# Optimization experiments

Measured on AMD Instinct MI355X. Metric: run time of the kernel, lower is better.

Reference implementation:

```python
import jax, jax.numpy as jnp
import numpy as np

K = 3
STRIDE = 1
PADDING = 1


def _conv2d(x, w, b, stride, padding):
    out = jax.lax.conv_general_dilated(
        x, w, window_strides=(stride, stride),
        padding=[(padding, padding), (padding, padding)],
        dimension_numbers=('NCHW', 'OIHW', 'NCHW'))
    return out + b[None, :, None, None]


def _grid_sample_bilinear_zeros(x, grid):
    B, C, Hin, Win = x.shape
    gx = (grid[..., 0] + 1.0) * (Win * 0.5) - 0.5  # (B,Hg,Wg) pixel coords
    gy = (grid[..., 1] + 1.0) * (Hin * 0.5) - 0.5
    x0f = jnp.floor(gx)
    y0f = jnp.floor(gy)
    wx1 = gx - x0f  # bilinear weights
    wy1 = gy - y0f
    x0 = x0f.astype(jnp.int32)
    y0 = y0f.astype(jnp.int32)
    xf = x.reshape(B, C, Hin * Win)

    def gather(yi, xi):
        valid = (xi >= 0) & (xi < Win) & (yi >= 0) & (yi < Hin)  # zero padding
        idx = jnp.clip(yi, 0, Hin - 1) * Win + jnp.clip(xi, 0, Win - 1)
        g = jax.vmap(lambda xb, ib: xb[:, ib])(xf, idx)  # (B,C,Hg,Wg)
        return g * valid[:, None, :, :].astype(x.dtype)

    w00 = ((1.0 - wx1) * (1.0 - wy1))[:, None]
    w01 = (wx1 * (1.0 - wy1))[:, None]
    w10 = ((1.0 - wx1) * wy1)[:, None]
    w11 = (wx1 * wy1)[:, None]
    return (gather(y0, x0) * w00 + gather(y0, x0 + 1) * w01 +
            gather(y0 + 1, x0) * w10 + gather(y0 + 1, x0 + 1) * w11)


def setup_inputs() -> dict:
    key = jax.random.key(0)
    k1, k2, k3 = jax.random.split(key, 3)
    B, C, O, H, W = 8, 128, 128, 64, 64
    x = jax.random.normal(k1, (B, C, H, W), dtype=jnp.float32)
    # small offset-predictor weights so sampled locations stay near the grid
    w_off = jax.random.normal(k2, (2 * K * K, C, K, K), dtype=jnp.float32) * 1e-3
    b_off = jnp.zeros((2 * K * K,), dtype=jnp.float32)
    w_main = jax.random.normal(k3, (O, C, K, K), dtype=jnp.float32) * 0.05
    b_main = jnp.zeros((O,), dtype=jnp.float32)
    return {"x": x, "w_off": w_off, "b_off": b_off, "w_main": w_main, "b_main": b_main}


def reference(x, w_off, b_off, w_main, b_main):
    offset = _conv2d(x, w_off, b_off, STRIDE, PADDING)  # (B, 2*K*K, H, W)
    B, _, H, W = offset.shape
    off = jnp.transpose(offset, (0, 2, 3, 1)).reshape(B, H, W, K, K, 2)
    # The torch in-place loops reduce to:
    #   x-comp: cumsum over i of column j=0, broadcast over j
    #   y-comp: cumsum over j of row    i=0, broadcast over i
    ox = jnp.cumsum(off[:, :, :, :, 0, 0], axis=3)  # (B,H,W,K)
    oy = jnp.cumsum(off[:, :, :, 0, :, 1], axis=3)  # (B,H,W,K)
    ox_f = jnp.broadcast_to(ox[..., None], (B, H, W, K, K))
    oy_f = jnp.broadcast_to(oy[:, :, :, None, :], (B, H, W, K, K))
    off_f = jnp.stack([ox_f, oy_f], axis=-1).reshape(B, H, W, K * K, 2)

    y_range = jnp.linspace(-1.0, 1.0, H, dtype=x.dtype)
    x_range = jnp.linspace(-1.0, 1.0, W, dtype=x.dtype)
    yg, xg = jnp.meshgrid(y_range, x_range, indexing='ij')
    base = jnp.stack((xg, yg), axis=-1)  # (H,W,2)
    grid = base[None, :, :, None, :] + off_f  # (B,H,W,K*K,2)
    grid = grid.reshape(B, H, W * K * K, 2)

    xs = _grid_sample_bilinear_zeros(x, grid)  # (B,C,H,W*K*K)
    C = x.shape[1]
    xs = xs.reshape(B, C, H, W, K * K)
    wm = w_main.reshape(w_main.shape[0], C, K * K)
    out = jnp.einsum('bchwk,ock->bohw', xs, wm)
    return out + b_main[None, :, None, None]
```

## Files before the change

### kernel.cpp

```cpp
#include <hip/hip_runtime.h>
#include <hip/hip_bf16.h>
#include <stdint.h>

typedef unsigned short u16;
typedef unsigned int u32;
typedef __attribute__((ext_vector_type(8))) short short8;
typedef __attribute__((ext_vector_type(4))) float float4v;
typedef __attribute__((ext_vector_type(2))) float float2v;

#define CH 128
#define OO 128
#define KD 1152
#define MPIX 32768

__device__ __forceinline__ u16 f2bf(float v) {
    __hip_bfloat16 h = __float2bfloat16(v);
    return *reinterpret_cast<u16*>(&h);
}

__device__ __forceinline__ float bf_lo(u32 u) {
    u32 t = u << 16;
    return __builtin_bit_cast(float, t);
}
__device__ __forceinline__ float bf_hi(u32 u) {
    u32 t = u & 0xffff0000u;
    return __builtin_bit_cast(float, t);
}
__device__ __forceinline__ float2v unpk(u32 u) {
    float2v r;
    r.x = bf_lo(u);
    r.y = bf_hi(u);
    return r;
}
__device__ __forceinline__ u32 pack_bf16(float lo, float hi) {
    return (u32)f2bf(lo) | ((u32)f2bf(hi) << 16);
}

__global__ __launch_bounds__(256) void prep_kernel(const float* __restrict__ x,
                                                   const float* __restrict__ w_off,
                                                   const float* __restrict__ w_main,
                                                   __hip_bfloat16* __restrict__ xt,
                                                   float* __restrict__ partial,
                                                   u16* __restrict__ Wb) {
    __shared__ float st[64][65];
    int tid = threadIdx.x;
    int bid = blockIdx.x;

    if (bid < 512) {
        int bh = bid;
        int b = bh >> 6;
        int h = bh & 63;
        const float* xb = x + ((size_t)b * CH) * 4096 + (size_t)h * 64;
        u32* xo32 = (u32*)(xt + ((size_t)bh << 6) * CH);
        for (int cc0 = 0; cc0 < 128; cc0 += 64) {
            #pragma unroll
            for (int step = 0; step < 16; ++step) {
                int cl = (tid >> 6) + step * 4;
                int w = tid & 63;
                st[cl][w] = xb[(size_t)(cc0 + cl) * 4096 + w];
            }
            __syncthreads();
            #pragma unroll
            for (int step = 0; step < 8; ++step) {
                int w = (tid >> 5) + step * 8;
                int p = tid & 31;
                u32 pair = pack_bf16(st[2 * p][w], st[2 * p + 1][w]);
                xo32[(size_t)w * 64 + (cc0 >> 1) + p] = pair;
            }
            __syncthreads();
        }
    } else if (bid < 1024) {
        int idx = bid - 512;
        int m = (idx & 127) * 256 + tid;
        int chunk = idx >> 7;
        int b = m >> 12;
        int hw = m & 4095;
        int h = hw >> 6;
        int w = hw & 63;
        float acc[6] = {0.f, 0.f, 0.f, 0.f, 0.f, 0.f};
        int c0 = chunk * 32;
        for (int c = c0; c < c0 + 32; ++c) {
            const float* xc = x + ((size_t)(b * CH + c) << 12);
            float xv[9];
            #pragma unroll
            for (int dy = 0; dy < 3; ++dy) {
                int yy = h + dy - 1;
                bool vy = (unsigned)yy < 64u;
                #pragma unroll
                for (int dx = 0; dx < 3; ++dx) {
                    int xx = w + dx - 1;
                    bool vv = vy && ((unsigned)xx < 64u);
                    xv[dy * 3 + dx] = vv ? xc[yy * 64 + xx] : 0.f;
                }
            }
            const float* wb = w_off + (size_t)c * 9;
            #pragma unroll
            for (int s = 0; s < 6; ++s) {
                int chn = (s < 3) ? s * 6 : (s - 3) * 2 + 1;
                const float* wp = wb + (size_t)chn * (CH * 9);
                float a = acc[s];
                #pragma unroll
                for (int t = 0; t < 9; ++t) a = fmaf(xv[t], wp[t], a);
                acc[s] = a;
            }
        }
        float* po = partial + ((size_t)(chunk << 15) + m) * 6;
        #pragma unroll
        for (int s = 0; s < 6; ++s) po[s] = acc[s];
    } else {
        int idx = (bid - 1024) * 256 + tid;
        if (idx < OO * KD) {
            int o = idx / KD;
            int r = idx - o * KD;
            int k = r >> 7;
            int c = r & 127;
            Wb[idx] = f2bf(w_main[(size_t)o * KD + c * 9 + k]);
        }
    }
}

__global__ __launch_bounds__(256) void fused_gemm_kernel(const __hip_bfloat16* __restrict__ xt,
                                                         const float* __restrict__ partial,
                                                         const float* __restrict__ b_off,
                                                         const u16* __restrict__ Wb,
                                                         const float* __restrict__ b_main,
                                                         float* __restrict__ out) {
    __shared__ float offs[64][6];
    __shared__ __align__(16) float4v twt[64][9];
    __shared__ __align__(16) int4 tbs[64][9];
    __shared__ __align__(16) u16 lB[2][64 * 32];

    int tid = threadIdx.x;
    int orig = blockIdx.x;
    int b = orig & 7;
    int h = orig >> 3;
    int m0 = ((b << 6) + h) << 6;

    for (int idx = tid; idx < 64 * 6; idx += 256) {
        int pix = idx / 6, s = idx % 6;
        int m = m0 + pix;
        int chn = (s < 3) ? s * 6 : (s - 3) * 2 + 1;
        float v = b_off[chn];
        #pragma unroll
        for (int q = 0; q < 4; ++q) v += partial[((size_t)(q << 15) + m) * 6 + s];
        offs[pix][s] = v;
    }
    __syncthreads();

    for (int idx = tid; idx < 64 * 9; idx += 256) {
        int pix = idx / 9, k = idx % 9;
        int i = k / 3, j = k - i * 3;
        float ox = offs[pix][0];
        if (i >= 1) ox += offs[pix][1];
        if (i >= 2) ox += offs[pix][2];
        float oy = offs[pix][3];
        if (j >= 1) oy += offs[pix][4];
        if (j >= 2) oy += offs[pix][5];
        const float step = 2.0f / 63.0f;
        float bxn = -1.0f + pix * step;
        float byn = -1.0f + h * step;
        float gx = fmaf(bxn + ox, 32.0f, 31.5f);
        float gy = fmaf(byn + oy, 32.0f, 31.5f);
        float x0f = floorf(gx), y0f = floorf(gy);
        float wx = gx - x0f, wy = gy - y0f;
        int ix0 = (int)x0f, iy0 = (int)y0f;
        int ix1 = ix0 + 1, iy1 = iy0 + 1;
        float fx0 = ((unsigned)ix0 < 64u) ? 1.f : 0.f;
        float fx1 = ((unsigned)ix1 < 64u) ? 1.f : 0.f;
        float fy0 = ((unsigned)iy0 < 64u) ? 1.f : 0.f;
        float fy1 = ((unsigned)iy1 < 64u) ? 1.f : 0.f;
        float4v wv;
        wv[0] = (1.f - wy) * (1.f - wx) * fy0 * fx0;
        wv[1] = (1.f - wy) * wx * fy0 * fx1;
        wv[2] = wy * (1.f - wx) * fy1 * fx0;
        wv[3] = wy * wx * fy1 * fx1;
        int cx0 = min(max(ix0, 0), 63), cx1 = min(max(ix1, 0), 63);
        int cy0 = min(max(iy0, 0), 63), cy1 = min(max(iy1, 0), 63);
        twt[pix][k] = wv;
        tbs[pix][k] = make_int4((cy0 * 64 + cx0) * 64, (cy0 * 64 + cx1) * 64,
                                (cy1 * 64 + cx0) * 64, (cy1 * 64 + cx1) * 64);
    }
    __syncthreads();

    int wave = tid >> 6, lane = tid & 63;
    int wo = wave & 1;
    int wp = wave >> 1;
    int mrow = lane & 15;
    int q8 = (lane >> 4) * 8;

    int pix = tid >> 2;
    int cgp = (tid & 3) * 8;
    const u32* xb = (const u32*)(xt + (((size_t)b << 12) * (size_t)CH));
    const u16* arow = Wb + (size_t)(wo * 64 + mrow) * KD + q8;
    int bsto = pix * 32 + cgp;

    float4v acc[4][2];
    #pragma unroll
    for (int sm = 0; sm < 4; ++sm)
        #pragma unroll
        for (int sn = 0; sn < 2; ++sn)
            acc[sm][sn] = (float4v){0.f, 0.f, 0.f, 0.f};

    float4v wv;
    int4 bv;
    uint4 u00, u01, u10, u11;

    auto issueB = [&](int kk) {
        if ((kk & 3) == 0) {
            int k = kk >> 2;
            wv = twt[pix][k];
            bv = tbs[pix][k];
        }
        const u32* xc = xb + ((((kk & 3) << 5) + cgp) >> 1);
        u00 = *(const uint4*)(xc + bv.x);
        u01 = *(const uint4*)(xc + bv.y);
        u10 = *(const uint4*)(xc + bv.z);
        u11 = *(const uint4*)(xc + bv.w);
    };
    auto issueA = [&](int kk, uint4* dst) {
        const u16* ap = arow + kk * 32;
        #pragma unroll
        for (int s = 0; s < 4; ++s)
            dst[s] = *(const uint4*)(ap + (size_t)(s * 16) * KD);
    };

    auto dostep = [&](int kk, uint4* aC, uint4* aN) {
        u16* lBc = &lB[kk & 1][0];
        {
            const u32* p00 = (const u32*)&u00;
            const u32* p01 = (const u32*)&u01;
            const u32* p10 = (const u32*)&u10;
            const u32* p11 = (const u32*)&u11;
            u32 outp[4];
            #pragma unroll
            for (int q = 0; q < 4; ++q) {
                float2v p = unpk(p00[q]) * wv[0];
                p += unpk(p01[q]) * wv[1];
                p += unpk(p10[q]) * wv[2];
                p += unpk(p11[q]) * wv[3];
                outp[q] = pack_bf16(p.x, p.y);
            }
            *(uint4*)&lBc[bsto] = *(const uint4*)outp;
        }

        if (kk < 35) {
            issueB(kk + 1);
            issueA(kk + 1, aN);
        }

        __syncthreads();

        short8 bfv[2];
        #pragma unroll
        for (int s = 0; s < 2; ++s)
            bfv[s] = *(const short8*)&lBc[(wp * 32 + s * 16 + mrow) * 32 + q8];
        #pragma unroll
        for (int sm = 0; sm < 4; ++sm) {
            short8 af = __builtin_bit_cast(short8, aC[sm]);
            #pragma unroll
            for (int sn = 0; sn < 2; ++sn)
                acc[sm][sn] = __builtin_amdgcn_mfma_f32_16x16x32_bf16(af, bfv[sn],
                                                                     acc[sm][sn], 0, 0, 0);
        }
    };

    uint4 aP[4], aQ[4];
    issueB(0);
    issueA(0, aP);
    for (int t = 0; t < 18; ++t) {
        dostep(2 * t, aP, aQ);
        dostep(2 * t + 1, aQ, aP);
    }

    #pragma unroll
    for (int sm = 0; sm < 4; ++sm) {
        int o = wo * 64 + sm * 16 + (lane >> 4) * 4;
        #pragma unroll
        for (int sn = 0; sn < 2; ++sn) {
            int pcol = m0 + wp * 32 + sn * 16 + mrow;
            int rem = pcol & 4095;
            float* op = out + (((size_t)b * OO) << 12) + rem;
            #pragma unroll
            for (int r = 0; r < 4; ++r)
                op[(size_t)(o + r) << 12] = acc[sm][sn][r] + b_main[o + r];
        }
    }
}

extern "C" void kernel_launch(void* const* d_in, const int* in_sizes, int n_in,
                              void* d_out, int out_size, void* d_ws, size_t ws_size,
                              hipStream_t stream) {
    const float* x      = (const float*)d_in[0];
    const float* w_off  = (const float*)d_in[1];
    const float* b_off  = (const float*)d_in[2];
    const float* w_main = (const float*)d_in[3];
    const float* b_main = (const float*)d_in[4];
    float* out = (float*)d_out;

    char* ws = (char*)d_ws;
    __hip_bfloat16* xt = (__hip_bfloat16*)ws;
    float* partial = (float*)(ws + 8388608);
    u16* Wb   = (u16*)(ws + 8388608 + 3145728);

    prep_kernel<<<1600, 256, 0, stream>>>(x, w_off, w_main, xt, partial, Wb);
    fused_gemm_kernel<<<MPIX / 64, 256, 0, stream>>>(xt, partial, b_off, Wb, b_main, out);
}
```

Before: 143.0 us.

## Halve pixel tile per block and stage weight tiles through LDS

The fused GEMM block now covers 32 pixels instead of 64, which doubles the grid to 1024 blocks. The weight (A) operand is loaded cooperatively into double-buffered LDS instead of each wave loading its own rows from global memory. Only half the threads build the bilinear-sampled B tile, and a launch bound of 4 blocks per CU is added to raise occupancy. The cost is that weights are re-read from L2 twice as often overall, and each step does more LDS traffic and synchronisation for fewer MFMAs.

```diff
diff --git a/kernel.cpp b/kernel.cpp
--- a/kernel.cpp
+++ b/kernel.cpp
@@ -119,25 +119,28 @@
     }
 }
 
-__global__ __launch_bounds__(256) void fused_gemm_kernel(const __hip_bfloat16* __restrict__ xt,
-                                                         const float* __restrict__ partial,
-                                                         const float* __restrict__ b_off,
-                                                         const u16* __restrict__ Wb,
-                                                         const float* __restrict__ b_main,
-                                                         float* __restrict__ out) {
-    __shared__ float offs[64][6];
-    __shared__ __align__(16) float4v twt[64][9];
-    __shared__ __align__(16) int4 tbs[64][9];
-    __shared__ __align__(16) u16 lB[2][64 * 32];
+__global__ __launch_bounds__(256, 4) void fused_gemm_kernel(const __hip_bfloat16* __restrict__ xt,
+                                                            const float* __restrict__ partial,
+                                                            const float* __restrict__ b_off,
+                                                            const u16* __restrict__ Wb,
+                                                            const float* __restrict__ b_main,
+                                                            float* __restrict__ out) {
+    __shared__ float offs[32][6];
+    __shared__ __align__(16) float4v twt[32][9];
+    __shared__ __align__(16) int4 tbs[32][9];
+    __shared__ __align__(16) u16 lA[2][128 * 32];
+    __shared__ __align__(16) u16 lB[2][32 * 32];
 
     int tid = threadIdx.x;
     int orig = blockIdx.x;
     int b = orig & 7;
-    int h = orig >> 3;
-    int m0 = ((b << 6) + h) << 6;
-
-    for (int idx = tid; idx < 64 * 6; idx += 256) {
-        int pix = idx / 6, s = idx % 6;
+    int idx = orig >> 3;
+    int h = idx >> 1;
+    int w0 = (idx & 1) << 5;
+    int m0 = (((b << 6) + h) << 6) + w0;
+
+    if (tid < 192) {
+        int pix = tid / 6, s = tid % 6;
         int m = m0 + pix;
         int chn = (s < 3) ? s * 6 : (s - 3) * 2 + 1;
         float v = b_off[chn];
@@ -147,8 +150,8 @@
     }
     __syncthreads();
 
-    for (int idx = tid; idx < 64 * 9; idx += 256) {
-        int pix = idx / 9, k = idx % 9;
+    for (int i2 = tid; i2 < 32 * 9; i2 += 256) {
+        int pix = i2 / 9, k = i2 % 9;
         int i = k / 3, j = k - i * 3;
         float ox = offs[pix][0];
         if (i >= 1) ox += offs[pix][1];
@@ -157,7 +160,7 @@
         if (j >= 1) oy += offs[pix][4];
         if (j >= 2) oy += offs[pix][5];
         const float step = 2.0f / 63.0f;
-        float bxn = -1.0f + pix * step;
+        float bxn = -1.0f + (w0 + pix) * step;
         float byn = -1.0f + h * step;
         float gx = fmaf(bxn + ox, 32.0f, 31.5f);
         float gy = fmaf(byn + oy, 32.0f, 31.5f);
@@ -183,20 +186,24 @@
     __syncthreads();
 
     int wave = tid >> 6, lane = tid & 63;
-    int wo = wave & 1;
-    int wp = wave >> 1;
     int mrow = lane & 15;
     int q8 = (lane >> 4) * 8;
 
-    int pix = tid >> 2;
+    int ar = tid >> 2;
+    int ag = (tid & 3) * 8;
+    const u16* aptr0 = Wb + (size_t)ar * KD + ag;
+    const u16* aptr1 = aptr0 + (size_t)64 * KD;
+    int asto = ar * 32 + ag;
+
+    int pixB = tid >> 2;
     int cgp = (tid & 3) * 8;
     const u32* xb = (const u32*)(xt + (((size_t)b << 12) * (size_t)CH));
-    const u16* arow = Wb + (size_t)(wo * 64 + mrow) * KD + q8;
-    int bsto = pix * 32 + cgp;
-
-    float4v acc[4][2];
+    int bsto = (tid >> 2 & 31) * 32 + cgp;
+    bool bstager = tid < 128;
+
+    float4v acc[2][2];
     #pragma unroll
-    for (int sm = 0; sm < 4; ++sm)
+    for (int sm = 0; sm < 2; ++sm)
         #pragma unroll
         for (int sn = 0; sn < 2; ++sn)
             acc[sm][sn] = (float4v){0.f, 0.f, 0.f, 0.f};
@@ -208,8 +215,8 @@
     auto issueB = [&](int kk) {
         if ((kk & 3) == 0) {
             int k = kk >> 2;
-            wv = twt[pix][k];
-            bv = tbs[pix][k];
+            wv = twt[pixB][k];
+            bv = tbs[pixB][k];
         }
         const u32* xc = xb + ((((kk & 3) << 5) + cgp) >> 1);
         u00 = *(const uint4*)(xc + bv.x);
@@ -218,15 +225,17 @@
         u11 = *(const uint4*)(xc + bv.w);
     };
     auto issueA = [&](int kk, uint4* dst) {
-        const u16* ap = arow + kk * 32;
-        #pragma unroll
-        for (int s = 0; s < 4; ++s)
-            dst[s] = *(const uint4*)(ap + (size_t)(s * 16) * KD);
+        dst[0] = *(const uint4*)(aptr0 + kk * 32);
+        dst[1] = *(const uint4*)(aptr1 + kk * 32);
     };
 
     auto dostep = [&](int kk, uint4* aC, uint4* aN) {
+        u16* lAc = &lA[kk & 1][0];
         u16* lBc = &lB[kk & 1][0];
-        {
+
+        *(uint4*)&lAc[asto] = aC[0];
+        *(uint4*)&lAc[asto + 64 * 32] = aC[1];
+        if (bstager) {
             const u32* p00 = (const u32*)&u00;
             const u32* p01 = (const u32*)&u01;
             const u32* p10 = (const u32*)&u10;
@@ -244,40 +253,41 @@
         }
 
         if (kk < 35) {
-            issueB(kk + 1);
             issueA(kk + 1, aN);
+            if (bstager) issueB(kk + 1);
         }
 
         __syncthreads();
 
-        short8 bfv[2];
+        short8 af[2], bfv[2];
         #pragma unroll
         for (int s = 0; s < 2; ++s)
-            bfv[s] = *(const short8*)&lBc[(wp * 32 + s * 16 + mrow) * 32 + q8];
-        #pragma unroll
-        for (int sm = 0; sm < 4; ++sm) {
-            short8 af = __builtin_bit_cast(short8, aC[sm]);
+            af[s] = *(const short8*)&lAc[(wave * 32 + s * 16 + mrow) * 32 + q8];
+        #pragma unroll
+        for (int s = 0; s < 2; ++s)
+            bfv[s] = *(const short8*)&lBc[(s * 16 + mrow) * 32 + q8];
+        #pragma unroll
+        for (int sm = 0; sm < 2; ++sm)
             #pragma unroll
             for (int sn = 0; sn < 2; ++sn)
-                acc[sm][sn] = __builtin_amdgcn_mfma_f32_16x16x32_bf16(af, bfv[sn],
+                acc[sm][sn] = __builtin_amdgcn_mfma_f32_16x16x32_bf16(af[sm], bfv[sn],
                                                                      acc[sm][sn], 0, 0, 0);
-        }
     };
 
-    uint4 aP[4], aQ[4];
-    issueB(0);
+    uint4 aP[2], aQ[2];
     issueA(0, aP);
+    if (bstager) issueB(0);
     for (int t = 0; t < 18; ++t) {
         dostep(2 * t, aP, aQ);
         dostep(2 * t + 1, aQ, aP);
     }
 
     #pragma unroll
-    for (int sm = 0; sm < 4; ++sm) {
-        int o = wo * 64 + sm * 16 + (lane >> 4) * 4;
+    for (int sm = 0; sm < 2; ++sm) {
+        int o = wave * 32 + sm * 16 + (lane >> 4) * 4;
         #pragma unroll
         for (int sn = 0; sn < 2; ++sn) {
-            int pcol = m0 + wp * 32 + sn * 16 + mrow;
+            int pcol = m0 + sn * 16 + mrow;
             int rem = pcol & 4095;
             float* op = out + (((size_t)b * OO) << 12) + rem;
             #pragma unroll
@@ -303,5 +313,5 @@
     u16* Wb   = (u16*)(ws + 8388608 + 3145728);
 
     prep_kernel<<<1600, 256, 0, stream>>>(x, w_off, w_main, xt, partial, Wb);
-    fused_gemm_kernel<<<MPIX / 64, 256, 0, stream>>>(xt, partial, b_off, Wb, b_main, out);
-}
+    fused_gemm_kernel<<<MPIX / 32, 256, 0, stream>>>(xt, partial, b_off, Wb, b_main, out);
+}
```

Measured after the change: 192.7 us. 1.35x slower.

## Stage weights through LDS and gather a full tap per burst

Applied to the files above, without the earlier changes.

The main fused GEMM kernel is restructured. Weight tiles are now loaded cooperatively into double-buffered LDS instead of each wave reading its own A fragments from global memory. The bilinear gather now fetches all 128 channels of one tap in a single burst, blends it into a padded LDS B tile (row stride 136), and overlaps that blend with the MFMA steps of the previous tap. Launch bounds now request two blocks per CU. The cost is more LDS, more registers held in flight for the 16 gather loads, and an extra barrier per k-step.

```diff
diff --git a/kernel.cpp b/kernel.cpp
--- a/kernel.cpp
+++ b/kernel.cpp
@@ -12,6 +12,7 @@
 #define OO 128
 #define KD 1152
 #define MPIX 32768
+#define LDBp 136
 
 __device__ __forceinline__ u16 f2bf(float v) {
     __hip_bfloat16 h = __float2bfloat16(v);
@@ -119,16 +120,17 @@
     }
 }
 
-__global__ __launch_bounds__(256) void fused_gemm_kernel(const __hip_bfloat16* __restrict__ xt,
-                                                         const float* __restrict__ partial,
-                                                         const float* __restrict__ b_off,
-                                                         const u16* __restrict__ Wb,
-                                                         const float* __restrict__ b_main,
-                                                         float* __restrict__ out) {
+__global__ __launch_bounds__(256, 2) void fused_gemm_kernel(const __hip_bfloat16* __restrict__ xt,
+                                                            const float* __restrict__ partial,
+                                                            const float* __restrict__ b_off,
+                                                            const u16* __restrict__ Wb,
+                                                            const float* __restrict__ b_main,
+                                                            float* __restrict__ out) {
     __shared__ float offs[64][6];
     __shared__ __align__(16) float4v twt[64][9];
     __shared__ __align__(16) int4 tbs[64][9];
-    __shared__ __align__(16) u16 lB[2][64 * 32];
+    __shared__ __align__(16) u16 lA[2][128 * 32];
+    __shared__ __align__(16) u16 lB[2][64 * LDBp];
 
     int tid = threadIdx.x;
     int orig = blockIdx.x;
@@ -147,8 +149,8 @@
     }
     __syncthreads();
 
-    for (int idx = tid; idx < 64 * 9; idx += 256) {
-        int pix = idx / 9, k = idx % 9;
+    for (int i2 = tid; i2 < 64 * 9; i2 += 256) {
+        int pix = i2 / 9, k = i2 % 9;
         int i = k / 3, j = k - i * 3;
         float ox = offs[pix][0];
         if (i >= 1) ox += offs[pix][1];
@@ -188,11 +190,17 @@
     int mrow = lane & 15;
     int q8 = (lane >> 4) * 8;
 
-    int pix = tid >> 2;
-    int cgp = (tid & 3) * 8;
+    int ar = tid >> 2;
+    int ag = (tid & 3) * 8;
+    const u16* aptr0 = Wb + (size_t)ar * KD + ag;
+    const u16* aptr1 = aptr0 + (size_t)64 * KD;
+    int asto = ar * 32 + ag;
+
+    int pixB = tid >> 2;
+    int t4 = tid & 3;
+    int t4o = t4 * 4;
     const u32* xb = (const u32*)(xt + (((size_t)b << 12) * (size_t)CH));
-    const u16* arow = Wb + (size_t)(wo * 64 + mrow) * KD + q8;
-    int bsto = pix * 32 + cgp;
+    int bwb = pixB * LDBp + t4 * 8;
 
     float4v acc[4][2];
     #pragma unroll
@@ -203,73 +211,107 @@
 
     float4v wv;
     int4 bv;
-    uint4 u00, u01, u10, u11;
-
-    auto issueB = [&](int kk) {
-        if ((kk & 3) == 0) {
-            int k = kk >> 2;
-            wv = twt[pix][k];
-            bv = tbs[pix][k];
-        }
-        const u32* xc = xb + ((((kk & 3) << 5) + cgp) >> 1);
-        u00 = *(const uint4*)(xc + bv.x);
-        u01 = *(const uint4*)(xc + bv.y);
-        u10 = *(const uint4*)(xc + bv.z);
-        u11 = *(const uint4*)(xc + bv.w);
+    uint4 u[4][4];
+
+    auto burst = [&](int t) {
+        wv = twt[pixB][t];
+        bv = tbs[pixB][t];
+        #pragma unroll
+        for (int q = 0; q < 4; ++q) {
+            u[0][q] = *(const uint4*)(xb + bv.x + q * 16 + t4o);
+            u[1][q] = *(const uint4*)(xb + bv.y + q * 16 + t4o);
+            u[2][q] = *(const uint4*)(xb + bv.z + q * 16 + t4o);
+            u[3][q] = *(const uint4*)(xb + bv.w + q * 16 + t4o);
+        }
     };
-    auto issueA = [&](int kk, uint4* dst) {
-        const u16* ap = arow + kk * 32;
-        #pragma unroll
-        for (int s = 0; s < 4; ++s)
-            dst[s] = *(const uint4*)(ap + (size_t)(s * 16) * KD);
+
+    auto blendq = [&](const uint4& a0, const uint4& a1, const uint4& a2,
+                      const uint4& a3, int col, u16* lBw) {
+        const u32* p00 = (const u32*)&a0;
+        const u32* p01 = (const u32*)&a1;
+        const u32* p10 = (const u32*)&a2;
+        const u32* p11 = (const u32*)&a3;
+        u32 outp[4];
+        #pragma unroll
+        for (int j = 0; j < 4; ++j) {
+            float2v p = unpk(p00[j]) * wv[0];
+            p += unpk(p01[j]) * wv[1];
+            p += unpk(p10[j]) * wv[2];
+            p += unpk(p11[j]) * wv[3];
+            outp[j] = pack_bf16(p.x, p.y);
+        }
+        *(uint4*)&lBw[bwb + col] = *(const uint4*)outp;
     };
 
-    auto dostep = [&](int kk, uint4* aC, uint4* aN) {
-        u16* lBc = &lB[kk & 1][0];
-        {
-            const u32* p00 = (const u32*)&u00;
-            const u32* p01 = (const u32*)&u01;
-            const u32* p10 = (const u32*)&u10;
-            const u32* p11 = (const u32*)&u11;
-            u32 outp[4];
-            #pragma unroll
-            for (int q = 0; q < 4; ++q) {
-                float2v p = unpk(p00[q]) * wv[0];
-                p += unpk(p01[q]) * wv[1];
-                p += unpk(p10[q]) * wv[2];
-                p += unpk(p11[q]) * wv[3];
-                outp[q] = pack_bf16(p.x, p.y);
-            }
-            *(uint4*)&lBc[bsto] = *(const uint4*)outp;
-        }
-
-        if (kk < 35) {
-            issueB(kk + 1);
-            issueA(kk + 1, aN);
-        }
-
+    auto stepA = [&](int kk, uint4& c0, uint4& c1, uint4& n0, uint4& n1, u16* lAc) {
+        *(uint4*)&lAc[asto] = c0;
+        *(uint4*)&lAc[asto + 64 * 32] = c1;
+        if (kk + 1 < 36) {
+            n0 = *(const uint4*)(aptr0 + (size_t)(kk + 1) * 32);
+            n1 = *(const uint4*)(aptr1 + (size_t)(kk + 1) * 32);
+        }
+    };
+
+    auto mfma_step = [&](const u16* lAc, const u16* lBr, int col) {
+        short8 af[4], bfv[2];
+        #pragma unroll
+        for (int i = 0; i < 4; ++i)
+            af[i] = *(const short8*)&lAc[(wo * 64 + i * 16 + mrow) * 32 + q8];
+        #pragma unroll
+        for (int sn = 0; sn < 2; ++sn)
+            bfv[sn] = *(const short8*)&lBr[(wp * 32 + sn * 16 + mrow) * LDBp + col + q8];
+        #pragma unroll
+        for (int i = 0; i < 4; ++i)
+            #pragma unroll
+            for (int sn = 0; sn < 2; ++sn)
+                acc[i][sn] = __builtin_amdgcn_mfma_f32_16x16x32_bf16(af[i], bfv[sn],
+                                                                    acc[i][sn], 0, 0, 0);
+    };
+
+    uint4 aC0 = *(const uint4*)aptr0;
+    uint4 aC1 = *(const uint4*)aptr1;
+    uint4 aN0, aN1;
+    burst(0);
+    {
+        u16* lBw = &lB[0][0];
+        blendq(u[0][0], u[1][0], u[2][0], u[3][0], 0,  lBw);
+        blendq(u[0][1], u[1][1], u[2][1], u[3][1], 32, lBw);
+        blendq(u[0][2], u[1][2], u[2][2], u[3][2], 64, lBw);
+        blendq(u[0][3], u[1][3], u[2][3], u[3][3], 96, lBw);
+    }
+
+    for (int t = 0; t < 9; ++t) {
+        int kk = t * 4;
+        const u16* lBr = &lB[t & 1][0];
+        u16* lBw = &lB[(t + 1) & 1][0];
+        u16* lA0 = &lA[0][0];
+        u16* lA1 = &lA[1][0];
+        bool more = t < 8;
+
+        if (more) burst(t + 1);
+        stepA(kk, aC0, aC1, aN0, aN1, lA0);
         __syncthreads();
-
-        short8 bfv[2];
-        #pragma unroll
-        for (int s = 0; s < 2; ++s)
-            bfv[s] = *(const short8*)&lBc[(wp * 32 + s * 16 + mrow) * 32 + q8];
-        #pragma unroll
-        for (int sm = 0; sm < 4; ++sm) {
-            short8 af = __builtin_bit_cast(short8, aC[sm]);
-            #pragma unroll
-            for (int sn = 0; sn < 2; ++sn)
-                acc[sm][sn] = __builtin_amdgcn_mfma_f32_16x16x32_bf16(af, bfv[sn],
-                                                                     acc[sm][sn], 0, 0, 0);
-        }
-    };
-
-    uint4 aP[4], aQ[4];
-    issueB(0);
-    issueA(0, aP);
-    for (int t = 0; t < 18; ++t) {
-        dostep(2 * t, aP, aQ);
-        dostep(2 * t + 1, aQ, aP);
+        mfma_step(lA0, lBr, 0);
+
+        stepA(kk + 1, aN0, aN1, aC0, aC1, lA1);
+        __syncthreads();
+        mfma_step(lA1, lBr, 32);
+
+        stepA(kk + 2, aC0, aC1, aN0, aN1, lA0);
+        if (more) {
+            blendq(u[0][0], u[1][0], u[2][0], u[3][0], 0,  lBw);
+            blendq(u[0][1], u[1][1], u[2][1], u[3][1], 32, lBw);
+        }
+        __syncthreads();
+        mfma_step(lA0, lBr, 64);
+
+        stepA(kk + 3, aN0, aN1, aC0, aC1, lA1);
+        if (more) {
+            blendq(u[0][2], u[1][2], u[2][2], u[3][2], 64, lBw);
+            blendq(u[0][3], u[1][3], u[2][3], u[3][3], 96, lBw);
+        }
+        __syncthreads();
+        mfma_step(lA1, lBr, 96);
     }
 
     #pragma unroll
```

Result: faster. 126.5 us (-11.6%).
